# Performance work log

Hardware: AMD Instinct MI355X
Metric: run time of the kernel (lower is better)

## Reference

```python
import jax, jax.numpy as jnp
import numpy as np

B, S, D = 8, 4096, 256
L, H = 4, 8
HD = D // H  # head_dim = 32
EPS = 1e-5


def layer_norm(x, gamma, beta):
    mu = jnp.mean(x, axis=-1, keepdims=True)
    var = jnp.mean(jnp.square(x - mu), axis=-1, keepdims=True)
    return (x - mu) * jax.lax.rsqrt(var + EPS) * gamma + beta


def setup_inputs() -> dict:
    key = jax.random.key(0)
    ks = jax.random.split(key, 9)
    sc = 0.02
    x = jax.random.normal(ks[0], (B, S, D), dtype=jnp.float32)
    # per-head projection weights, torch Linear convention: (out=head_dim, in=D)
    Wq = jax.random.normal(ks[1], (L, H, HD, D), dtype=jnp.float32) * sc
    Wk = jax.random.normal(ks[2], (L, H, HD, D), dtype=jnp.float32) * sc
    Wv = jax.random.normal(ks[3], (L, H, HD, D), dtype=jnp.float32) * sc
    W1 = jax.random.normal(ks[4], (L, D, D), dtype=jnp.float32) * sc
    b1 = jax.random.normal(ks[5], (L, D), dtype=jnp.float32) * sc
    W2 = jax.random.normal(ks[6], (L, D, D), dtype=jnp.float32) * sc
    b2 = jax.random.normal(ks[7], (L, D), dtype=jnp.float32) * sc
    gamma = jnp.ones((D,), dtype=jnp.float32)
    beta = jnp.zeros((D,), dtype=jnp.float32)
    return {"processed_grid_repr": x, "Wq": Wq, "Wk": Wk, "Wv": Wv,
            "W1": W1, "b1": b1, "W2": W2, "b2": b2,
            "gamma": gamma, "beta": beta}


def reference(processed_grid_repr, Wq, Wk, Wv, W1, b1, W2, b2, gamma, beta):
    out = processed_grid_repr  # (B, S, D)
    scale = 1.0 / jnp.sqrt(jnp.float32(S))  # original scales by sqrt(seq_len)
    for l in range(L):
        h = layer_norm(out, gamma, beta)
        # all heads at once: (B, H, S, HD)
        Q = jnp.einsum('bsd,hed->bhse', h, Wq[l])
        K = jnp.einsum('bsd,hed->bhse', h, Wk[l])
        V = jnp.einsum('bsd,hed->bhse', h, Wv[l])
        # original does key.reshape(B, HD, S) (a RESHAPE, not a transpose)
        Kr = K.reshape(B, H, HD, S)
        # original einsum 'bqq,bqd->bqd' only uses the diagonal of QK^r,
        # so compute only the diagonal: diag[b,h,q] = sum_e Q[b,h,q,e]*Kr[b,h,e,q]
        diag = jnp.einsum('bhse,bhes->bhs', Q, Kr) * scale
        attn = diag[..., None] * V  # (B, H, S, HD)
        # concat heads along last dim (head order preserved)
        msa_out = attn.transpose(0, 2, 1, 3).reshape(B, S, D)
        attended = msa_out + out
        m = layer_norm(attended, gamma, beta)
        m = jax.nn.gelu(m @ W1[l].T + b1[l], approximate=False)
        m = jax.nn.gelu(m @ W2[l].T + b2[l], approximate=False)
        out = m + attended
    # final: layer norm of CLS-like token 0
    return layer_norm(out[:, 0, :], gamma, beta)  # (B, D)
```

## Files before the change

kernel.cpp:

```cpp
#include <hip/hip_runtime.h>
#include <hip/hip_bf16.h>
#include <hip/hip_fp16.h>

typedef _Float16 half_t;
typedef _Float16 half8 __attribute__((ext_vector_type(8)));
typedef _Float16 half4 __attribute__((ext_vector_type(4)));
typedef float f32x4 __attribute__((ext_vector_type(4)));

#define BB 8
#define SS 4096
#define DD 256
#define HH 8
#define LL 4
#define MTOT (BB*SS)

__device__ inline float gelu_f(float v) { return 0.5f * v * (1.0f + erff(v * 0.70710678118f)); }

__device__ __forceinline__ void gload16(const half_t* g, half_t* l) {
    __builtin_amdgcn_global_load_lds(
        (const __attribute__((address_space(1))) void*)g,
        (__attribute__((address_space(3))) void*)l, 16, 0, 0);
}

__global__ __launch_bounds__(256) void prep_weights(
    const float* __restrict__ Wq, const float* __restrict__ Wk, const float* __restrict__ Wv,
    const float* __restrict__ W1, const float* __restrict__ b1,
    const float* __restrict__ W2, const float* __restrict__ b2,
    const float* __restrict__ gamma, const float* __restrict__ beta,
    half_t* __restrict__ Wall, half_t* __restrict__ W1h, half_t* __restrict__ W2h,
    float* __restrict__ bqkv, float* __restrict__ b1f, float* __restrict__ b2f)
{
    int blk = blockIdx.x;
    int l = blk / 5, type = blk % 5;
    int o = threadIdx.x;
    const float* src = (type == 0 ? Wq : type == 1 ? Wk : type == 2 ? Wv : type == 3 ? W1 : W2)
                       + ((size_t)l * 256 + o) * 256;
    half_t* dsth = (type < 3) ? Wall + ((size_t)(l * 3 + type) * 256 + o) * 256
                 : (type == 3) ? W1h + ((size_t)l * 256 + o) * 256
                               : W2h + ((size_t)l * 256 + o) * 256;
    float acc = 0.f;
    for (int d4 = 0; d4 < 64; ++d4) {
        float4 w = *(const float4*)(src + d4 * 4);
        half4 hv;
        if (type == 4) {
            hv = half4{ (half_t)w.x, (half_t)w.y, (half_t)w.z, (half_t)w.w };
        } else {
            float4 g = *(const float4*)(gamma + d4 * 4);
            float4 bt = *(const float4*)(beta + d4 * 4);
            acc += w.x * bt.x + w.y * bt.y + w.z * bt.z + w.w * bt.w;
            hv = half4{ (half_t)(w.x * g.x), (half_t)(w.y * g.y), (half_t)(w.z * g.z), (half_t)(w.w * g.w) };
        }
        *(half4*)(dsth + d4 * 4) = hv;
    }
    if (type < 3) bqkv[(l * 3 + type) * 256 + o] = acc;
    else if (type == 3) b1f[l * 256 + o] = b1[l * 256 + o] + acc;
    else b2f[l * 256 + o] = b2[l * 256 + o];
}

__global__ __launch_bounds__(256) void cvt_x(const float* __restrict__ in, half_t* __restrict__ out) {
    int i = (blockIdx.x * 256 + threadIdx.x) * 4;
    float4 v = *(const float4*)(in + i);
    half4 h = { (half_t)v.x, (half_t)v.y, (half_t)v.z, (half_t)v.w };
    *(half4*)(out + i) = h;
}

__global__ __launch_bounds__(256) void ln_z(const half_t* __restrict__ in, half_t* __restrict__ z) {
    int wave = threadIdx.x >> 6, lane = threadIdx.x & 63;
    int row = blockIdx.x * 4 + wave;
    size_t base = (size_t)row * DD + lane * 4;
    half4 x4 = *(const half4*)(in + base);
    float a0 = x4[0], a1 = x4[1], a2 = x4[2], a3 = x4[3];
    float s1 = a0 + a1 + a2 + a3;
    float s2 = a0 * a0 + a1 * a1 + a2 * a2 + a3 * a3;
    #pragma unroll
    for (int m = 32; m; m >>= 1) {
        s1 += __shfl_xor(s1, m);
        s2 += __shfl_xor(s2, m);
    }
    float mu = s1 * (1.0f / DD);
    float var = s2 * (1.0f / DD) - mu * mu;
    float rs = rsqrtf(var + 1e-5f);
    half4 o = { (half_t)((a0 - mu) * rs), (half_t)((a1 - mu) * rs),
                (half_t)((a2 - mu) * rs), (half_t)((a3 - mu) * rs) };
    *(half4*)(z + base) = o;
}

__device__ inline void xcd_remap(int& bx, int& by, int& bz) {
    int lin = blockIdx.x + gridDim.x * (blockIdx.y + gridDim.y * blockIdx.z);
    int nyz = gridDim.y * gridDim.z;
    int xcd = lin & 7;
    int slot = lin >> 3;
    int yz = slot % nyz;
    int xi = slot / nyz;
    bx = xcd + 8 * xi;
    by = yz % gridDim.y;
    bz = yz / gridDim.y;
}

template<int EPI>
__global__ __launch_bounds__(256) void gemm128(const half_t* __restrict__ A,
                                               const half_t* __restrict__ Wbase,
                                               const float* __restrict__ biasBase,
                                               const half_t* __restrict__ resid,
                                               half_t* __restrict__ o0,
                                               half_t* __restrict__ o1,
                                               half_t* __restrict__ o2) {
    const int t = threadIdx.x, lane = t & 63, wavei = t >> 6;
    const int wm = wavei >> 1, wn = wavei & 1, r = lane & 15, g = lane >> 4;
    int bx, by, bz;
    xcd_remap(bx, by, bz);
    const int row0 = bx * 128, col0 = by * 128;
    const half_t* W = Wbase + (size_t)bz * 65536;
    const float* bias = biasBase + bz * 256;
    half_t* outp = (bz == 0) ? o0 : ((bz == 1) ? o1 : o2);

    __shared__ __align__(16) half_t lds[2][16384];

    const half_t* Ag = A + (size_t)row0 * DD;
    const half_t* Wg = W + (size_t)col0 * DD;

    int rowS[4], chS[4];
    #pragma unroll
    for (int i = 0; i < 4; ++i) {
        int G = i * 256 + t;
        rowS[i] = G >> 3;
        chS[i] = ((G & 7) ^ (rowS[i] & 7)) * 8;
    }

    #pragma unroll
    for (int i = 0; i < 4; ++i) {
        int G = i * 256 + t;
        gload16(Ag + (size_t)rowS[i] * DD + chS[i], &lds[0][G * 8]);
        gload16(Wg + (size_t)rowS[i] * DD + chS[i], &lds[0][8192 + G * 8]);
    }
    __syncthreads();

    f32x4 acc[4][4];
    #pragma unroll
    for (int i = 0; i < 4; ++i)
        #pragma unroll
        for (int j = 0; j < 4; ++j) acc[i][j] = (f32x4){0.f, 0.f, 0.f, 0.f};

    #pragma unroll
    for (int stp = 0; stp < 4; ++stp) {
        const int cur = stp & 1;
        if (stp < 3) {
            int kk = (stp + 1) * 64;
            #pragma unroll
            for (int i = 0; i < 4; ++i) {
                int G = i * 256 + t;
                gload16(Ag + (size_t)rowS[i] * DD + kk + chS[i], &lds[cur ^ 1][G * 8]);
                gload16(Wg + (size_t)rowS[i] * DD + kk + chS[i], &lds[cur ^ 1][8192 + G * 8]);
            }
        }
        #pragma unroll
        for (int ks = 0; ks < 2; ++ks) {
            half8 af[4], bf[4];
            #pragma unroll
            for (int mt = 0; mt < 4; ++mt) {
                int rw = wm * 64 + mt * 16 + r;
                int cc = (ks * 4 + g) ^ (rw & 7);
                af[mt] = *(const half8*)&lds[cur][rw * 64 + cc * 8];
            }
            #pragma unroll
            for (int nt = 0; nt < 4; ++nt) {
                int rw = wn * 64 + nt * 16 + r;
                int cc = (ks * 4 + g) ^ (rw & 7);
                bf[nt] = *(const half8*)&lds[cur][8192 + rw * 64 + cc * 8];
            }
            #pragma unroll
            for (int mt = 0; mt < 4; ++mt)
                #pragma unroll
                for (int nt = 0; nt < 4; ++nt)
                    acc[mt][nt] = __builtin_amdgcn_mfma_f32_16x16x32_f16(af[mt], bf[nt], acc[mt][nt], 0, 0, 0);
        }
        __syncthreads();
    }

    half_t* ldsT = &lds[0][0];
    #pragma unroll
    for (int mt = 0; mt < 4; ++mt) {
        #pragma unroll
        for (int nt = 0; nt < 4; ++nt) {
            int colL = wn * 64 + nt * 16 + r;
            float bv = bias[col0 + colL];
            #pragma unroll
            for (int j = 0; j < 4; ++j) {
                int rowL = wm * 64 + mt * 16 + g * 4 + j;
                float v = acc[mt][nt][j] + bv;
                if (EPI != 0) v = gelu_f(v);
                ldsT[rowL * 128 + (colL ^ ((rowL & 12) << 2))] = (half_t)v;
            }
        }
    }
    __syncthreads();
    const int l15 = lane & 15, lg = lane >> 4;
    #pragma unroll
    for (int i = 0; i < 8; ++i) {
        int rowL = wavei * 32 + lg * 8 + i;
        int colL = l15 * 8;
        half8 v = *(const half8*)&ldsT[rowL * 128 + (colL ^ ((rowL & 12) << 2))];
        size_t off = (size_t)(row0 + rowL) * DD + col0 + colL;
        if (EPI == 2) {
            half8 rsd = *(const half8*)&resid[off];
            #pragma unroll
            for (int q = 0; q < 8; ++q) v[q] = (half_t)((float)v[q] + (float)rsd[q]);
        }
        *(half8*)&outp[off] = v;
    }
}

__global__ __launch_bounds__(256) void diag_tiled(const half_t* __restrict__ Q,
                                                  const half_t* __restrict__ K,
                                                  float* __restrict__ dg) {
    int blk = blockIdx.x;
    int sblk = blk & 15, h = (blk >> 4) & 7, b = blk >> 7;
    int t = threadIdx.x;
    __shared__ __align__(16) half_t kt[256 * 32];
    int r0b = sblk * 8;
    {
        int e = t >> 3, del = t & 7;
        const half_t* kp = K + ((size_t)b * SS + e * 128 + r0b + del) * DD + h * 32;
        int4* dst = (int4*)&kt[t * 32];
        const int4* sp = (const int4*)kp;
        dst[0] = sp[0]; dst[1] = sp[1]; dst[2] = sp[2]; dst[3] = sp[3];
    }
    __syncthreads();
    int s = sblk * 256 + t;
    const half8* q8 = (const half8*)(Q + ((size_t)b * SS + s) * DD + h * 32);
    int cs = t & 31, ds = t >> 5;
    float sum = 0.f;
    #pragma unroll
    for (int v = 0; v < 4; ++v) {
        half8 qq = q8[v];
        #pragma unroll
        for (int j = 0; j < 8; ++j) {
            int e = v * 8 + j;
            sum += (float)qq[j] * (float)kt[(e * 8 + ds) * 32 + cs];
        }
    }
    dg[((size_t)b << 15) | ((size_t)h << 12) | s] = sum * 0.015625f;
}

__global__ __launch_bounds__(256) void attn_ln16(const half_t* __restrict__ resid,
                                                 const half_t* __restrict__ V,
                                                 const float* __restrict__ dg,
                                                 half_t* __restrict__ att,
                                                 half_t* __restrict__ z2) {
    int wave = threadIdx.x >> 6, lane = threadIdx.x & 63;
    int row = blockIdx.x * 4 + wave;
    int b = row >> 12, s = row & (SS - 1);
    int h = lane >> 3;
    float dgv = dg[((size_t)b << 15) | ((size_t)h << 12) | s];
    size_t base = (size_t)row * DD + lane * 4;
    half4 rs4 = *(const half4*)(resid + base);
    half4 v4 = *(const half4*)(V + base);
    float a0 = (float)rs4[0] + dgv * (float)v4[0];
    float a1 = (float)rs4[1] + dgv * (float)v4[1];
    float a2 = (float)rs4[2] + dgv * (float)v4[2];
    float a3 = (float)rs4[3] + dgv * (float)v4[3];
    half4 at = { (half_t)a0, (half_t)a1, (half_t)a2, (half_t)a3 };
    *(half4*)(att + base) = at;
    float s1 = a0 + a1 + a2 + a3;
    float s2 = a0 * a0 + a1 * a1 + a2 * a2 + a3 * a3;
    #pragma unroll
    for (int m = 32; m; m >>= 1) {
        s1 += __shfl_xor(s1, m);
        s2 += __shfl_xor(s2, m);
    }
    float mu = s1 * (1.0f / DD);
    float var = s2 * (1.0f / DD) - mu * mu;
    float rsq = rsqrtf(var + 1e-5f);
    half4 o = { (half_t)((a0 - mu) * rsq), (half_t)((a1 - mu) * rsq),
                (half_t)((a2 - mu) * rsq), (half_t)((a3 - mu) * rsq) };
    *(half4*)(z2 + base) = o;
}

__global__ __launch_bounds__(256) void final_ln_kernel(const half_t* __restrict__ cur,
                                                       float* __restrict__ out,
                                                       const float* __restrict__ gamma,
                                                       const float* __restrict__ beta) {
    int b = blockIdx.x;
    int d = threadIdx.x;
    float x = (float)cur[(size_t)b * SS * DD + d];
    float s1 = x, s2 = x * x;
    #pragma unroll
    for (int m = 32; m; m >>= 1) {
        s1 += __shfl_xor(s1, m);
        s2 += __shfl_xor(s2, m);
    }
    __shared__ float ls1[4], ls2[4];
    int wave = threadIdx.x >> 6, lane = threadIdx.x & 63;
    if (lane == 0) { ls1[wave] = s1; ls2[wave] = s2; }
    __syncthreads();
    float t1 = ls1[0] + ls1[1] + ls1[2] + ls1[3];
    float t2 = ls2[0] + ls2[1] + ls2[2] + ls2[3];
    float mu = t1 * (1.0f / DD);
    float var = t2 * (1.0f / DD) - mu * mu;
    float rs = rsqrtf(var + 1e-5f);
    out[(size_t)b * DD + d] = (x - mu) * rs * gamma[d] + beta[d];
}

extern "C" void kernel_launch(void* const* d_in, const int* in_sizes, int n_in,
                              void* d_out, int out_size, void* d_ws, size_t ws_size,
                              hipStream_t stream) {
    const float* x     = (const float*)d_in[0];
    const float* Wq    = (const float*)d_in[1];
    const float* Wk    = (const float*)d_in[2];
    const float* Wv    = (const float*)d_in[3];
    const float* W1    = (const float*)d_in[4];
    const float* b1    = (const float*)d_in[5];
    const float* W2    = (const float*)d_in[6];
    const float* b2    = (const float*)d_in[7];
    const float* gamma = (const float*)d_in[8];
    const float* beta  = (const float*)d_in[9];

    char* p = (char*)d_ws;
    half_t* x16  = (half_t*)p; p += (size_t)MTOT * DD * 2;
    half_t* cur  = (half_t*)p; p += (size_t)MTOT * DD * 2;
    half_t* att  = (half_t*)p; p += (size_t)MTOT * DD * 2;
    half_t* z1   = (half_t*)p; p += (size_t)MTOT * DD * 2;
    half_t* z2   = (half_t*)p; p += (size_t)MTOT * DD * 2;
    half_t* Qb   = (half_t*)p; p += (size_t)MTOT * DD * 2;
    half_t* Kb   = (half_t*)p; p += (size_t)MTOT * DD * 2;
    half_t* Vb   = (half_t*)p; p += (size_t)MTOT * DD * 2;
    half_t* m1   = (half_t*)p; p += (size_t)MTOT * DD * 2;
    float*  dgp  = (float*)p;  p += (size_t)BB * HH * SS * 4;
    half_t* Wall = (half_t*)p; p += (size_t)LL * 3 * 65536 * 2;
    half_t* W1h  = (half_t*)p; p += (size_t)LL * 65536 * 2;
    half_t* W2h  = (half_t*)p; p += (size_t)LL * 65536 * 2;
    float*  bqkv = (float*)p;  p += (size_t)LL * 3 * 256 * 4;
    float*  b1f  = (float*)p;  p += (size_t)LL * 256 * 4;
    float*  b2f  = (float*)p;  p += (size_t)LL * 256 * 4;

    prep_weights<<<LL * 5, 256, 0, stream>>>(Wq, Wk, Wv, W1, b1, W2, b2, gamma, beta,
                                             Wall, W1h, W2h, bqkv, b1f, b2f);
    cvt_x<<<8192, 256, 0, stream>>>(x, x16);

    const half_t* curin = x16;
    for (int l = 0; l < LL; ++l) {
        ln_z<<<MTOT / 4, 256, 0, stream>>>(curin, z1);
        gemm128<0><<<dim3(256, 2, 3), 256, 0, stream>>>(
            z1, Wall + (size_t)l * 3 * 65536, bqkv + l * 3 * 256, nullptr, Qb, Kb, Vb);
        diag_tiled<<<1024, 256, 0, stream>>>(Qb, Kb, dgp);
        attn_ln16<<<MTOT / 4, 256, 0, stream>>>(curin, Vb, dgp, att, z2);
        gemm128<1><<<dim3(256, 2, 1), 256, 0, stream>>>(
            z2, W1h + (size_t)l * 65536, b1f + l * 256, nullptr, m1, m1, m1);
        gemm128<2><<<dim3(256, 2, 1), 256, 0, stream>>>(
            m1, W2h + (size_t)l * 65536, b2f + l * 256, att, cur, cur, cur);
        curin = cur;
    }
    final_ln_kernel<<<BB, 256, 0, stream>>>(cur, (float*)d_out, gamma, beta);
}
```

Baseline: 367.6 us.

## Fold LayerNorm normalization into GEMM A-operand load using per-row stats

LayerNorm kernels now compute only per-row mean and rsqrt and write them out as small float2 stats, instead of writing a full normalized fp16 copy of the activations. The QKV and first MLP GEMMs read the raw residual and attended activations and apply (x*rs - mu*rs) in fp16 on the A fragments right after each LDS read. This removes two full-size activation writes and reads per layer. In exchange it adds a packed FMA per A fragment inside the MFMA loop. It also changes rounding, since normalization now runs in fp16 arithmetic rather than fp32.

Result: no change. 369.7 us (+0.6%).

```diff
diff --git a/kernel.cpp b/kernel.cpp
--- a/kernel.cpp
+++ b/kernel.cpp
@@ -15,6 +15,7 @@
 #define MTOT (BB*SS)
 
 __device__ inline float gelu_f(float v) { return 0.5f * v * (1.0f + erff(v * 0.70710678118f)); }
+__device__ inline half8 splat8(half_t v) { return (half8){v, v, v, v, v, v, v, v}; }
 
 __device__ __forceinline__ void gload16(const half_t* g, half_t* l) {
     __builtin_amdgcn_global_load_lds(
@@ -64,7 +65,8 @@
     *(half4*)(out + i) = h;
 }
 
-__global__ __launch_bounds__(256) void ln_z(const half_t* __restrict__ in, half_t* __restrict__ z) {
+__global__ __launch_bounds__(256) void row_stats(const half_t* __restrict__ in,
+                                                 float2* __restrict__ st) {
     int wave = threadIdx.x >> 6, lane = threadIdx.x & 63;
     int row = blockIdx.x * 4 + wave;
     size_t base = (size_t)row * DD + lane * 4;
@@ -77,12 +79,11 @@
         s1 += __shfl_xor(s1, m);
         s2 += __shfl_xor(s2, m);
     }
-    float mu = s1 * (1.0f / DD);
-    float var = s2 * (1.0f / DD) - mu * mu;
-    float rs = rsqrtf(var + 1e-5f);
-    half4 o = { (half_t)((a0 - mu) * rs), (half_t)((a1 - mu) * rs),
-                (half_t)((a2 - mu) * rs), (half_t)((a3 - mu) * rs) };
-    *(half4*)(z + base) = o;
+    if (lane == 0) {
+        float mu = s1 * (1.0f / DD);
+        float var = s2 * (1.0f / DD) - mu * mu;
+        st[row] = make_float2(mu, rsqrtf(var + 1e-5f));
+    }
 }
 
 __device__ inline void xcd_remap(int& bx, int& by, int& bz) {
@@ -97,8 +98,9 @@
     bz = yz / gridDim.y;
 }
 
-template<int EPI>
+template<int NORM, int EPI>
 __global__ __launch_bounds__(256) void gemm128(const half_t* __restrict__ A,
+                                               const float2* __restrict__ statsA,
                                                const half_t* __restrict__ Wbase,
                                                const float* __restrict__ biasBase,
                                                const half_t* __restrict__ resid,
@@ -119,6 +121,16 @@
     const half_t* Ag = A + (size_t)row0 * DD;
     const half_t* Wg = W + (size_t)col0 * DD;
 
+    half8 sA[4], bA[4];
+    if (NORM) {
+        #pragma unroll
+        for (int mt = 0; mt < 4; ++mt) {
+            float2 st = statsA[row0 + wm * 64 + mt * 16 + r];
+            sA[mt] = splat8((half_t)st.y);
+            bA[mt] = splat8((half_t)(-st.x * st.y));
+        }
+    }
+
     int rowS[4], chS[4];
     #pragma unroll
     for (int i = 0; i < 4; ++i) {
@@ -160,7 +172,8 @@
             for (int mt = 0; mt < 4; ++mt) {
                 int rw = wm * 64 + mt * 16 + r;
                 int cc = (ks * 4 + g) ^ (rw & 7);
-                af[mt] = *(const half8*)&lds[cur][rw * 64 + cc * 8];
+                half8 raw = *(const half8*)&lds[cur][rw * 64 + cc * 8];
+                af[mt] = NORM ? (half8)(raw * sA[mt] + bA[mt]) : raw;
             }
             #pragma unroll
             for (int nt = 0; nt < 4; ++nt) {
@@ -242,11 +255,11 @@
     dg[((size_t)b << 15) | ((size_t)h << 12) | s] = sum * 0.015625f;
 }
 
-__global__ __launch_bounds__(256) void attn_ln16(const half_t* __restrict__ resid,
+__global__ __launch_bounds__(256) void attn_stat(const half_t* __restrict__ resid,
                                                  const half_t* __restrict__ V,
                                                  const float* __restrict__ dg,
                                                  half_t* __restrict__ att,
-                                                 half_t* __restrict__ z2) {
+                                                 float2* __restrict__ st2) {
     int wave = threadIdx.x >> 6, lane = threadIdx.x & 63;
     int row = blockIdx.x * 4 + wave;
     int b = row >> 12, s = row & (SS - 1);
@@ -268,12 +281,11 @@
         s1 += __shfl_xor(s1, m);
         s2 += __shfl_xor(s2, m);
     }
-    float mu = s1 * (1.0f / DD);
-    float var = s2 * (1.0f / DD) - mu * mu;
-    float rsq = rsqrtf(var + 1e-5f);
-    half4 o = { (half_t)((a0 - mu) * rsq), (half_t)((a1 - mu) * rsq),
-                (half_t)((a2 - mu) * rsq), (half_t)((a3 - mu) * rsq) };
-    *(half4*)(z2 + base) = o;
+    if (lane == 0) {
+        float mu = s1 * (1.0f / DD);
+        float var = s2 * (1.0f / DD) - mu * mu;
+        st2[row] = make_float2(mu, rsqrtf(var + 1e-5f));
+    }
 }
 
 __global__ __launch_bounds__(256) void final_ln_kernel(const half_t* __restrict__ cur,
@@ -319,13 +331,13 @@
     half_t* x16  = (half_t*)p; p += (size_t)MTOT * DD * 2;
     half_t* cur  = (half_t*)p; p += (size_t)MTOT * DD * 2;
     half_t* att  = (half_t*)p; p += (size_t)MTOT * DD * 2;
-    half_t* z1   = (half_t*)p; p += (size_t)MTOT * DD * 2;
-    half_t* z2   = (half_t*)p; p += (size_t)MTOT * DD * 2;
     half_t* Qb   = (half_t*)p; p += (size_t)MTOT * DD * 2;
     half_t* Kb   = (half_t*)p; p += (size_t)MTOT * DD * 2;
     half_t* Vb   = (half_t*)p; p += (size_t)MTOT * DD * 2;
     half_t* m1   = (half_t*)p; p += (size_t)MTOT * DD * 2;
     float*  dgp  = (float*)p;  p += (size_t)BB * HH * SS * 4;
+    float2* stA  = (float2*)p; p += (size_t)MTOT * 8;
+    float2* stB  = (float2*)p; p += (size_t)MTOT * 8;
     half_t* Wall = (half_t*)p; p += (size_t)LL * 3 * 65536 * 2;
     half_t* W1h  = (half_t*)p; p += (size_t)LL * 65536 * 2;
     half_t* W2h  = (half_t*)p; p += (size_t)LL * 65536 * 2;
@@ -339,15 +351,15 @@
 
     const half_t* curin = x16;
     for (int l = 0; l < LL; ++l) {
-        ln_z<<<MTOT / 4, 256, 0, stream>>>(curin, z1);
-        gemm128<0><<<dim3(256, 2, 3), 256, 0, stream>>>(
-            z1, Wall + (size_t)l * 3 * 65536, bqkv + l * 3 * 256, nullptr, Qb, Kb, Vb);
+        row_stats<<<MTOT / 4, 256, 0, stream>>>(curin, stA);
+        gemm128<1, 0><<<dim3(256, 2, 3), 256, 0, stream>>>(
+            curin, stA, Wall + (size_t)l * 3 * 65536, bqkv + l * 3 * 256, nullptr, Qb, Kb, Vb);
         diag_tiled<<<1024, 256, 0, stream>>>(Qb, Kb, dgp);
-        attn_ln16<<<MTOT / 4, 256, 0, stream>>>(curin, Vb, dgp, att, z2);
-        gemm128<1><<<dim3(256, 2, 1), 256, 0, stream>>>(
-            z2, W1h + (size_t)l * 65536, b1f + l * 256, nullptr, m1, m1, m1);
-        gemm128<2><<<dim3(256, 2, 1), 256, 0, stream>>>(
-            m1, W2h + (size_t)l * 65536, b2f + l * 256, att, cur, cur, cur);
+        attn_stat<<<MTOT / 4, 256, 0, stream>>>(curin, Vb, dgp, att, stB);
+        gemm128<1, 1><<<dim3(256, 2, 1), 256, 0, stream>>>(
+            att, stB, W1h + (size_t)l * 65536, b1f + l * 256, nullptr, m1, m1, m1);
+        gemm128<0, 2><<<dim3(256, 2, 1), 256, 0, stream>>>(
+            m1, nullptr, W2h + (size_t)l * 65536, b2f + l * 256, att, cur, cur, cur);
         curin = cur;
     }
     final_ln_kernel<<<BB, 256, 0, stream>>>(cur, (float*)d_out, gamma, beta);
```
